# Kernel tuning notes

Hardware: AMD Instinct MI355X
Metric: run time of the kernel (lower is better)

Reference implementation:

```python
import jax, jax.numpy as jnp
import numpy as np

DIM = 256
HEADS = 4
DIM_HEADS = 32
HIDDEN = HEADS * DIM_HEADS


def setup_inputs() -> dict:
    key = jax.random.key(0)
    k0, k1, k2, k3, k4, k5, k6 = jax.random.split(key, 7)
    b, c, h, w = 16, DIM, 64, 64
    s = 1.0 / np.sqrt(DIM)
    return {
        "x": jax.random.normal(k0, (b, c, h, w), dtype=jnp.float32),
        "Wq": jax.random.normal(k1, (HIDDEN, DIM), dtype=jnp.float32) * s,
        "Wk": jax.random.normal(k2, (HIDDEN, DIM), dtype=jnp.float32) * s,
        "Wv": jax.random.normal(k3, (HIDDEN, DIM), dtype=jnp.float32) * s,
        "Wo": jax.random.normal(k4, (DIM, HIDDEN), dtype=jnp.float32) / np.sqrt(HIDDEN),
        "bo": jax.random.normal(k5, (DIM,), dtype=jnp.float32) * 0.01,
        "g": jnp.ones((DIM,), dtype=jnp.float32),
    }


def reference(x, Wq, Wk, Wv, Wo, bo, g):
    b, c, h, w = x.shape
    n = h * w
    scale = DIM_HEADS ** (-0.5)
    xf = x.reshape(b, c, n)  # [b,c,n]
    # 1x1 convs == channel matmuls
    q = jnp.einsum('dc,bcn->bdn', Wq, xf).reshape(b, HEADS, DIM_HEADS, n)
    k = jnp.einsum('dc,bcn->bdn', Wk, xf).reshape(b, HEADS, DIM_HEADS, n)
    v = jnp.einsum('dc,bcn->bdn', Wv, xf).reshape(b, HEADS, DIM_HEADS, n)
    q = jax.nn.softmax(q, axis=-2) * scale  # softmax over head-dim
    k = jax.nn.softmax(k, axis=-1)          # softmax over tokens
    v = v / n
    context = jnp.einsum('bhdn,bhen->bhde', k, v)  # [b,h,dh,dh]
    out = jnp.einsum('bhde,bhdn->bhen', context, q)  # [b,h,dh,n]
    out = out.reshape(b, HIDDEN, n)
    out = jnp.einsum('cd,bdn->bcn', Wo, out) + bo[None, :, None]
    # LayerNorm over channel dim (biased var, eps=1e-5 for fp32)
    eps = 1e-5
    mean = jnp.mean(out, axis=1, keepdims=True)
    var = jnp.var(out, axis=1, keepdims=True)
    out = (out - mean) * jax.lax.rsqrt(var + eps) * g[None, :, None]
    return out.reshape(b, c, h, w)
```

## Files before the change

kernel.cpp:

```cpp
#include <hip/hip_runtime.h>
#include <hip/hip_bf16.h>

typedef float f32x4 __attribute__((ext_vector_type(4)));
typedef short bf16x8 __attribute__((ext_vector_type(8)));
typedef unsigned short us4 __attribute__((ext_vector_type(4)));
typedef unsigned short us8 __attribute__((ext_vector_type(8)));

#define NB 16
#define NC 256
#define NTOK 4096
#define NHID 128

#define APAD 264
#define PK 68
#define PQ 132

__device__ __forceinline__ unsigned short f2bf(float f) {
  union { float f; unsigned u; } v; v.f = f;
  return (unsigned short)((v.u + 0x7fffu + ((v.u >> 16) & 1u)) >> 16);
}
__device__ __forceinline__ float bf2f(unsigned short h) {
  union { unsigned u; float f; } v; v.u = ((unsigned)h) << 16;
  return v.f;
}

__global__ __launch_bounds__(512) void k0_w(
    const float* __restrict__ Wq, const float* __restrict__ Wk,
    const float* __restrict__ Wv, unsigned short* __restrict__ Wswz)
{
  const int mt = blockIdx.x;
  const int t = threadIdx.x;
  const int ks = t >> 6, l = t & 63;
  const int m = mt * 16 + (l & 15);
  const int col = ks * 32 + (l >> 4) * 8;
  const float* src = (m < 128) ? (Wq + (size_t)m * NC)
                   : (m < 256) ? (Wk + (size_t)(m - 128) * NC)
                               : (Wv + (size_t)(m - 256) * NC);
  const float4 w0 = *(const float4*)(src + col);
  const float4 w1 = *(const float4*)(src + col + 4);
  us8 p;
  p[0] = f2bf(w0.x); p[1] = f2bf(w0.y); p[2] = f2bf(w0.z); p[3] = f2bf(w0.w);
  p[4] = f2bf(w1.x); p[5] = f2bf(w1.y); p[6] = f2bf(w1.z); p[7] = f2bf(w1.w);
  *(us8*)&Wswz[((size_t)(mt * 8 + ks)) * 512 + l * 8] = p;
}

__global__ __launch_bounds__(512, 4) void k1_qkv(
    const float* __restrict__ x, const unsigned short* __restrict__ Wswz,
    unsigned short* __restrict__ qswz, unsigned short* __restrict__ Pp,
    float* __restrict__ Sp)
{
  __shared__ __align__(16) unsigned char smem[51712];
  unsigned short* As = (unsigned short*)smem;
  unsigned short* postKV = (unsigned short*)smem;
  unsigned short* postQ = (unsigned short*)(smem + 34816);

  const int tile = blockIdx.x, b = blockIdx.y;
  const int n0 = tile * 64;
  const int t = threadIdx.x;
  const int wid = t >> 6, l = t & 63;
  const int l16 = l & 15, lhi = l >> 4;
  const int tokh = wid >> 2;
  const int mw = wid & 3;
  const int mb = mw * 96;

  {
    const int slot = t & 15;
    const int cp0 = t >> 4;
    const float* xb = x + ((size_t)b * NC) * NTOK + n0;
#pragma unroll
    for (int i = 0; i < 4; ++i) {
      const int c0 = 2 * (cp0 + 32 * i);
      const float4 a0 = *(const float4*)(xb + (size_t)c0 * NTOK + slot * 4);
      const float4 a1 = *(const float4*)(xb + (size_t)(c0 + 1) * NTOK + slot * 4);
      const float* p0 = (const float*)&a0;
      const float* p1 = (const float*)&a1;
#pragma unroll
      for (int j = 0; j < 4; ++j)
        *(unsigned*)&As[(slot * 4 + j) * APAD + c0] =
            (unsigned)f2bf(p0[j]) | ((unsigned)f2bf(p1[j]) << 16);
    }
  }
  __syncthreads();

  f32x4 acc[2][6];
#pragma unroll
  for (int i = 0; i < 2; ++i)
#pragma unroll
    for (int j = 0; j < 6; ++j) acc[i][j] = 0;

  const int mt0 = mw * 6;
  for (int ks = 0; ks < 8; ++ks) {
    bf16x8 af[2];
#pragma unroll
    for (int tf = 0; tf < 2; ++tf)
      af[tf] = *(const bf16x8*)&As[(tokh * 32 + tf * 16 + l16) * APAD + ks * 32 + lhi * 8];
#pragma unroll
    for (int nf = 0; nf < 6; ++nf) {
      const bf16x8 bfv = *(const bf16x8*)&Wswz[((size_t)((mt0 + nf) * 8 + ks)) * 512 + l * 8];
#pragma unroll
      for (int tf = 0; tf < 2; ++tf)
        acc[tf][nf] = __builtin_amdgcn_mfma_f32_16x16x32_bf16(af[tf], bfv, acc[tf][nf], 0, 0, 0);
    }
  }

  const float qscale = 0.1767766952966369f;
#pragma unroll
  for (int pr = 0; pr < 3; ++pr) {
    const int mg = mb + pr * 32;
    if (mg < 128) {
#pragma unroll
      for (int tf = 0; tf < 2; ++tf)
#pragma unroll
        for (int r = 0; r < 4; ++r) {
          const float a0 = acc[tf][2 * pr][r], a1 = acc[tf][2 * pr + 1][r];
          float mx = fmaxf(a0, a1);
          mx = fmaxf(mx, __shfl_xor(mx, 1));
          mx = fmaxf(mx, __shfl_xor(mx, 2));
          mx = fmaxf(mx, __shfl_xor(mx, 4));
          mx = fmaxf(mx, __shfl_xor(mx, 8));
          const float e0 = __expf(a0 - mx), e1 = __expf(a1 - mx);
          float s = e0 + e1;
          s += __shfl_xor(s, 1); s += __shfl_xor(s, 2);
          s += __shfl_xor(s, 4); s += __shfl_xor(s, 8);
          const float inv = qscale / s;
          acc[tf][2 * pr][r] = e0 * inv;
          acc[tf][2 * pr + 1][r] = e1 * inv;
        }
    } else if (mg < 256) {
#pragma unroll
      for (int f = 0; f < 2; ++f) {
        float s = 0.f;
#pragma unroll
        for (int tf = 0; tf < 2; ++tf)
#pragma unroll
          for (int r = 0; r < 4; ++r) {
            const float e = __expf(acc[tf][2 * pr + f][r]);
            acc[tf][2 * pr + f][r] = e;
            s += e;
          }
        s += __shfl_xor(s, 16);
        s += __shfl_xor(s, 32);
        if (l < 16)
          Sp[(((size_t)b * 64 + tile) * 2 + tokh) * 128 + (mg - 128) + f * 16 + l16] = s;
      }
    }
  }
  __syncthreads();

#pragma unroll
  for (int nf = 0; nf < 6; ++nf) {
    const int mg = mb + nf * 16;
    if (mg < 128) {
#pragma unroll
      for (int tf = 0; tf < 2; ++tf) {
        const int tok = tokh * 32 + tf * 16 + lhi * 4;
#pragma unroll
        for (int r = 0; r < 4; ++r)
          postQ[(tok + r) * PQ + mg + l16] = f2bf(acc[tf][nf][r]);
      }
    } else {
      const int row = mg - 128 + l16;
#pragma unroll
      for (int tf = 0; tf < 2; ++tf) {
        us4 p;
#pragma unroll
        for (int r = 0; r < 4; ++r) p[r] = f2bf(acc[tf][nf][r]);
        *(us4*)&postKV[row * PK + tokh * 32 + tf * 16 + lhi * 4] = p;
      }
    }
  }
  __syncthreads();

  if (wid >= 4) {
    const int h = wid - 4;
    f32x4 ca[2][2];
    ca[0][0] = 0; ca[0][1] = 0; ca[1][0] = 0; ca[1][1] = 0;
#pragma unroll
    for (int ks2 = 0; ks2 < 2; ++ks2) {
      bf16x8 ae[2], be[2];
#pragma unroll
      for (int d = 0; d < 2; ++d)
        ae[d] = *(const bf16x8*)&postKV[(h * 32 + d * 16 + l16) * PK + ks2 * 32 + lhi * 8];
#pragma unroll
      for (int e = 0; e < 2; ++e)
        be[e] = *(const bf16x8*)&postKV[(128 + h * 32 + e * 16 + l16) * PK + ks2 * 32 + lhi * 8];
#pragma unroll
      for (int d = 0; d < 2; ++d)
#pragma unroll
        for (int e = 0; e < 2; ++e)
          ca[d][e] = __builtin_amdgcn_mfma_f32_16x16x32_bf16(ae[d], be[e], ca[d][e], 0, 0, 0);
    }
    unsigned short* pb = Pp + (((size_t)b * 64 + tile) * 4 + h) * 1024;
#pragma unroll
    for (int d = 0; d < 2; ++d)
#pragma unroll
      for (int e = 0; e < 2; ++e) {
        us4 p;
#pragma unroll
        for (int r = 0; r < 4; ++r) p[r] = f2bf(ca[d][e][r]);
        *(us4*)&pb[(e * 16 + l16) * 32 + d * 16 + lhi * 4] = p;
      }
  } else {
    const int g = wid;
#pragma unroll
    for (int ks = 0; ks < 4; ++ks) {
      const bf16x8 v = *(const bf16x8*)&postQ[(g * 16 + l16) * PQ + ks * 32 + lhi * 8];
      *(bf16x8*)&qswz[(((size_t)(b * 256 + tile * 4 + g)) * 4 + ks) * 512 + l * 8] = v;
    }
  }
}

__global__ __launch_bounds__(256) void k2_reduce(
    const unsigned short* __restrict__ Pp, const float* __restrict__ Sp,
    float* __restrict__ Cn)
{
  __shared__ float Ss[32];
  const int h = blockIdx.x, b = blockIdx.y;
  const int t = threadIdx.x;
  if (t < 32) {
    float s = 0.f;
    const float* sb = Sp + (size_t)b * 16384 + h * 32 + t;
    for (int i = 0; i < 128; ++i) s += sb[i * 128];
    Ss[t] = 1.0f / (s * 4096.0f);
  }
  __syncthreads();
  const int e = t >> 3, d4 = (t & 7) * 4;
  f32x4 a = 0;
  for (int tile = 0; tile < 64; ++tile) {
    const us4 v = *(const us4*)&Pp[(((size_t)b * 64 + tile) * 4 + h) * 1024 + e * 32 + d4];
    a[0] += bf2f(v[0]); a[1] += bf2f(v[1]); a[2] += bf2f(v[2]); a[3] += bf2f(v[3]);
  }
  f32x4 o;
#pragma unroll
  for (int j = 0; j < 4; ++j) o[j] = a[j] * Ss[d4 + j];
  *(f32x4*)&Cn[(size_t)b * 4096 + h * 1024 + e * 32 + d4] = o;
}

__global__ __launch_bounds__(256) void k2_m(
    const float* __restrict__ Wo, const float* __restrict__ Cn,
    unsigned short* __restrict__ Mswz)
{
  const int ct = blockIdx.x, b = blockIdx.y;
  const int t = threadIdx.x;
  const int ks = t >> 6, l = t & 63;
  const int c = ct * 16 + (l & 15);
  const int d0 = (l >> 4) * 8;
  const float* wr = Wo + (size_t)c * NHID + ks * 32;
  const float* cb = Cn + (size_t)b * 4096 + ks * 1024;
  f32x4 s0 = 0, s1 = 0;
#pragma unroll 8
  for (int e = 0; e < 32; ++e) {
    const float w = wr[e];
    const f32x4 c0 = *(const f32x4*)&cb[e * 32 + d0];
    const f32x4 c1 = *(const f32x4*)&cb[e * 32 + d0 + 4];
#pragma unroll
    for (int j = 0; j < 4; ++j) { s0[j] += w * c0[j]; s1[j] += w * c1[j]; }
  }
  us8 p;
#pragma unroll
  for (int j = 0; j < 4; ++j) { p[j] = f2bf(s0[j]); p[4 + j] = f2bf(s1[j]); }
  *(us8*)&Mswz[(((size_t)b * 16 + ct) * 4 + ks) * 512 + l * 8] = p;
}

__global__ __launch_bounds__(256, 3) void k3_out(
    const unsigned short* __restrict__ qswz, const unsigned short* __restrict__ Mswz,
    const float* __restrict__ bo, const float* __restrict__ g, float* __restrict__ out)
{
  __shared__ float red[4 * 64 * 2];
  const int bx = blockIdx.x, b = blockIdx.y;
  const int t = threadIdx.x;
  const int wid = t >> 6, l = t & 63;
  const int l16 = l & 15, lhi = l >> 4;

  bf16x8 mf[4][4];
#pragma unroll
  for (int cf = 0; cf < 4; ++cf)
#pragma unroll
    for (int ks = 0; ks < 4; ++ks)
      mf[cf][ks] = *(const bf16x8*)&Mswz[(((size_t)b * 16 + wid * 4 + cf) * 4 + ks) * 512 + l * 8];

  f32x4 acc[4][4];
#pragma unroll
  for (int i = 0; i < 4; ++i)
#pragma unroll
    for (int j = 0; j < 4; ++j) acc[i][j] = 0;

#pragma unroll
  for (int tf = 0; tf < 4; ++tf) {
    bf16x8 qf[4];
#pragma unroll
    for (int ks = 0; ks < 4; ++ks)
      qf[ks] = *(const bf16x8*)&qswz[(((size_t)(b * 256 + bx * 4 + tf)) * 4 + ks) * 512 + l * 8];
#pragma unroll
    for (int ks = 0; ks < 4; ++ks)
#pragma unroll
      for (int cf = 0; cf < 4; ++cf)
        acc[tf][cf] = __builtin_amdgcn_mfma_f32_16x16x32_bf16(qf[ks], mf[cf][ks], acc[tf][cf], 0, 0, 0);
  }

  float bol[4], gl[4];
#pragma unroll
  for (int cf = 0; cf < 4; ++cf) {
    const int c = wid * 64 + cf * 16 + l16;
    bol[cf] = bo[c]; gl[cf] = g[c];
  }
#pragma unroll
  for (int tf = 0; tf < 4; ++tf)
#pragma unroll
    for (int cf = 0; cf < 4; ++cf)
#pragma unroll
      for (int r = 0; r < 4; ++r) acc[tf][cf][r] += bol[cf];

#pragma unroll
  for (int tf = 0; tf < 4; ++tf)
#pragma unroll
    for (int r = 0; r < 4; ++r) {
      float s = 0.f, q2 = 0.f;
#pragma unroll
      for (int cf = 0; cf < 4; ++cf) {
        const float v = acc[tf][cf][r];
        s += v; q2 += v * v;
      }
      s += __shfl_xor(s, 1); q2 += __shfl_xor(q2, 1);
      s += __shfl_xor(s, 2); q2 += __shfl_xor(q2, 2);
      s += __shfl_xor(s, 4); q2 += __shfl_xor(q2, 4);
      s += __shfl_xor(s, 8); q2 += __shfl_xor(q2, 8);
      if (l16 == 0) {
        const int tok = tf * 16 + lhi * 4 + r;
        red[(wid * 64 + tok) * 2] = s;
        red[(wid * 64 + tok) * 2 + 1] = q2;
      }
    }
  __syncthreads();

  float mean[4][4], rstd[4][4];
#pragma unroll
  for (int tf = 0; tf < 4; ++tf)
#pragma unroll
    for (int r = 0; r < 4; ++r) {
      const int tok = tf * 16 + lhi * 4 + r;
      float s = 0.f, q2 = 0.f;
#pragma unroll
      for (int cg = 0; cg < 4; ++cg) {
        s += red[(cg * 64 + tok) * 2];
        q2 += red[(cg * 64 + tok) * 2 + 1];
      }
      const float mu = s * (1.0f / 256.0f);
      const float var = q2 * (1.0f / 256.0f) - mu * mu;
      mean[tf][r] = mu;
      rstd[tf][r] = rsqrtf(var + 1e-5f);
    }

  float* ob = out + ((size_t)b * NC) * NTOK + bx * 64;
#pragma unroll
  for (int tf = 0; tf < 4; ++tf)
#pragma unroll
    for (int cf = 0; cf < 4; ++cf) {
      const int c = wid * 64 + cf * 16 + l16;
      f32x4 ov;
#pragma unroll
      for (int r = 0; r < 4; ++r)
        ov[r] = (acc[tf][cf][r] - mean[tf][r]) * rstd[tf][r] * gl[cf];
      *(f32x4*)&ob[(size_t)c * NTOK + tf * 16 + lhi * 4] = ov;
    }
}

extern "C" void kernel_launch(void* const* d_in, const int* in_sizes, int n_in,
                              void* d_out, int out_size, void* d_ws, size_t ws_size,
                              hipStream_t stream) {
  const float* x  = (const float*)d_in[0];
  const float* Wq = (const float*)d_in[1];
  const float* Wk = (const float*)d_in[2];
  const float* Wv = (const float*)d_in[3];
  const float* Wo = (const float*)d_in[4];
  const float* bo = (const float*)d_in[5];
  const float* g  = (const float*)d_in[6];
  float* out = (float*)d_out;

  char* ws = (char*)d_ws;
  unsigned short* Wswz = (unsigned short*)(ws);
  unsigned short* qswz = (unsigned short*)(ws + 262144);
  unsigned short* Pp   = (unsigned short*)(ws + 17039360);
  float*          Sp   = (float*)(ws + 25427968);
  float*          Cn   = (float*)(ws + 26476544);
  unsigned short* Mswz = (unsigned short*)(ws + 26738688);
  (void)ws_size; (void)in_sizes; (void)n_in; (void)out_size;

  hipLaunchKernelGGL(k0_w, dim3(24), dim3(512), 0, stream, Wq, Wk, Wv, Wswz);
  hipLaunchKernelGGL(k1_qkv, dim3(64, NB), dim3(512), 0, stream, x, Wswz, qswz, Pp, Sp);
  hipLaunchKernelGGL(k2_reduce, dim3(4, NB), dim3(256), 0, stream, Pp, Sp, Cn);
  hipLaunchKernelGGL(k2_m, dim3(16, NB), dim3(256), 0, stream, Wo, Cn, Mswz);
  hipLaunchKernelGGL(k3_out, dim3(64, NB), dim3(256), 0, stream, qswz, Mswz, bo, g, out);
}
```

Measured before the change: 92.16 us.

## Reassign QKV warp tiles, XOR-swizzle LDS layouts, use packed bf16 conversion

The QKV kernel now gives each warp all 64 tokens and three 16-row output fragments, so each Wswz fragment is fetched once per warp and the per-token-half split of key sums goes away. Padded LDS arrays are replaced by XOR-swizzled layouts, which shrink shared memory enough to raise the occupancy hint to 6 blocks. Manual bf16 rounding is replaced by the packed hardware conversion intrinsics. The risks are more accumulator registers per warp, which may not fit the new occupancy target, and an uneven softmax workload across warps.

```diff
diff --git a/kernel.cpp b/kernel.cpp
--- a/kernel.cpp
+++ b/kernel.cpp
@@ -4,20 +4,23 @@
 typedef float f32x4 __attribute__((ext_vector_type(4)));
 typedef short bf16x8 __attribute__((ext_vector_type(8)));
 typedef unsigned short us4 __attribute__((ext_vector_type(4)));
-typedef unsigned short us8 __attribute__((ext_vector_type(8)));
 
 #define NB 16
 #define NC 256
 #define NTOK 4096
 #define NHID 128
 
-#define APAD 264
-#define PK 68
-#define PQ 132
-
+__device__ __forceinline__ unsigned pk2(float lo, float hi) {
+  float2 f; f.x = lo; f.y = hi;
+  __hip_bfloat162 h = __float22bfloat162_rn(f);
+  unsigned u; __builtin_memcpy(&u, &h, 4); return u;
+}
 __device__ __forceinline__ unsigned short f2bf(float f) {
-  union { float f; unsigned u; } v; v.f = f;
-  return (unsigned short)((v.u + 0x7fffu + ((v.u >> 16) & 1u)) >> 16);
+  __hip_bfloat16 h = __float2bfloat16(f);
+  unsigned short u; __builtin_memcpy(&u, &h, 2); return u;
+}
+__device__ __forceinline__ uint2 pk4(f32x4 v) {
+  uint2 r; r.x = pk2(v[0], v[1]); r.y = pk2(v[2], v[3]); return r;
 }
 __device__ __forceinline__ float bf2f(unsigned short h) {
   union { unsigned u; float f; } v; v.u = ((unsigned)h) << 16;
@@ -38,30 +41,29 @@
                                : (Wv + (size_t)(m - 256) * NC);
   const float4 w0 = *(const float4*)(src + col);
   const float4 w1 = *(const float4*)(src + col + 4);
-  us8 p;
-  p[0] = f2bf(w0.x); p[1] = f2bf(w0.y); p[2] = f2bf(w0.z); p[3] = f2bf(w0.w);
-  p[4] = f2bf(w1.x); p[5] = f2bf(w1.y); p[6] = f2bf(w1.z); p[7] = f2bf(w1.w);
-  *(us8*)&Wswz[((size_t)(mt * 8 + ks)) * 512 + l * 8] = p;
-}
-
-__global__ __launch_bounds__(512, 4) void k1_qkv(
+  uint4 p;
+  p.x = pk2(w0.x, w0.y); p.y = pk2(w0.z, w0.w);
+  p.z = pk2(w1.x, w1.y); p.w = pk2(w1.z, w1.w);
+  *(uint4*)&Wswz[((size_t)(mt * 8 + ks)) * 512 + l * 8] = p;
+}
+
+__global__ __launch_bounds__(512, 6) void k1_qkv(
     const float* __restrict__ x, const unsigned short* __restrict__ Wswz,
     unsigned short* __restrict__ qswz, unsigned short* __restrict__ Pp,
     float* __restrict__ Sp)
 {
-  __shared__ __align__(16) unsigned char smem[51712];
-  unsigned short* As = (unsigned short*)smem;
-  unsigned short* postKV = (unsigned short*)smem;
-  unsigned short* postQ = (unsigned short*)(smem + 34816);
+  __shared__ __align__(16) unsigned char smem[49152];
 
   const int tile = blockIdx.x, b = blockIdx.y;
   const int n0 = tile * 64;
   const int t = threadIdx.x;
   const int wid = t >> 6, l = t & 63;
   const int l16 = l & 15, lhi = l >> 4;
-  const int tokh = wid >> 2;
-  const int mw = wid & 3;
-  const int mb = mw * 96;
+  const unsigned xr = (unsigned)((l16 & 7) << 4);
+
+  int fr[3];
+  if (wid < 4) { fr[0] = 2 * wid; fr[1] = 2 * wid + 1; fr[2] = 8 + wid; }
+  else { const int w = wid - 4; fr[0] = 12 + w; fr[1] = 16 + 2 * w; fr[2] = 17 + 2 * w; }
 
   {
     const int slot = t & 15;
@@ -75,98 +77,111 @@
       const float* p0 = (const float*)&a0;
       const float* p1 = (const float*)&a1;
 #pragma unroll
-      for (int j = 0; j < 4; ++j)
-        *(unsigned*)&As[(slot * 4 + j) * APAD + c0] =
-            (unsigned)f2bf(p0[j]) | ((unsigned)f2bf(p1[j]) << 16);
+      for (int j = 0; j < 4; ++j) {
+        const int tok = slot * 4 + j;
+        const unsigned off = (unsigned)(tok * 512 + 2 * c0) ^ ((unsigned)(tok & 7) << 4);
+        *(unsigned*)(smem + off) = pk2(p0[j], p1[j]);
+      }
     }
   }
   __syncthreads();
 
-  f32x4 acc[2][6];
-#pragma unroll
-  for (int i = 0; i < 2; ++i)
-#pragma unroll
-    for (int j = 0; j < 6; ++j) acc[i][j] = 0;
-
-  const int mt0 = mw * 6;
+  f32x4 acc[4][3];
+#pragma unroll
+  for (int i = 0; i < 4; ++i)
+#pragma unroll
+    for (int j = 0; j < 3; ++j) acc[i][j] = 0;
+
   for (int ks = 0; ks < 8; ++ks) {
-    bf16x8 af[2];
-#pragma unroll
-    for (int tf = 0; tf < 2; ++tf)
-      af[tf] = *(const bf16x8*)&As[(tokh * 32 + tf * 16 + l16) * APAD + ks * 32 + lhi * 8];
-#pragma unroll
-    for (int nf = 0; nf < 6; ++nf) {
-      const bf16x8 bfv = *(const bf16x8*)&Wswz[((size_t)((mt0 + nf) * 8 + ks)) * 512 + l * 8];
-#pragma unroll
-      for (int tf = 0; tf < 2; ++tf)
-        acc[tf][nf] = __builtin_amdgcn_mfma_f32_16x16x32_bf16(af[tf], bfv, acc[tf][nf], 0, 0, 0);
+    bf16x8 af[4];
+#pragma unroll
+    for (int tf = 0; tf < 4; ++tf)
+      af[tf] = *(const bf16x8*)(smem +
+          (((unsigned)((tf * 16 + l16) * 512 + ks * 64 + lhi * 16)) ^ xr));
+#pragma unroll
+    for (int f = 0; f < 3; ++f) {
+      const bf16x8 bfv = *(const bf16x8*)&Wswz[((size_t)(fr[f] * 8 + ks)) * 512 + l * 8];
+#pragma unroll
+      for (int tf = 0; tf < 4; ++tf)
+        acc[tf][f] = __builtin_amdgcn_mfma_f32_16x16x32_bf16(af[tf], bfv, acc[tf][f], 0, 0, 0);
     }
   }
 
   const float qscale = 0.1767766952966369f;
-#pragma unroll
-  for (int pr = 0; pr < 3; ++pr) {
-    const int mg = mb + pr * 32;
-    if (mg < 128) {
-#pragma unroll
-      for (int tf = 0; tf < 2; ++tf)
+  if (wid < 4) {
+#pragma unroll
+    for (int tf = 0; tf < 4; ++tf)
+#pragma unroll
+      for (int r = 0; r < 4; ++r) {
+        const float a0 = acc[tf][0][r], a1 = acc[tf][1][r];
+        float mx = fmaxf(a0, a1);
+        mx = fmaxf(mx, __shfl_xor(mx, 1));
+        mx = fmaxf(mx, __shfl_xor(mx, 2));
+        mx = fmaxf(mx, __shfl_xor(mx, 4));
+        mx = fmaxf(mx, __shfl_xor(mx, 8));
+        const float e0 = __expf(a0 - mx), e1 = __expf(a1 - mx);
+        float s = e0 + e1;
+        s += __shfl_xor(s, 1); s += __shfl_xor(s, 2);
+        s += __shfl_xor(s, 4); s += __shfl_xor(s, 8);
+        const float inv = qscale / s;
+        acc[tf][0][r] = e0 * inv;
+        acc[tf][1][r] = e1 * inv;
+      }
+    float s = 0.f;
+#pragma unroll
+    for (int tf = 0; tf < 4; ++tf)
+#pragma unroll
+      for (int r = 0; r < 4; ++r) {
+        const float e = __expf(acc[tf][2][r]);
+        acc[tf][2][r] = e;
+        s += e;
+      }
+    s += __shfl_xor(s, 16);
+    s += __shfl_xor(s, 32);
+    if (l < 16) Sp[((size_t)b * 64 + tile) * 128 + (fr[2] - 8) * 16 + l16] = s;
+  } else {
+    float s = 0.f;
+#pragma unroll
+    for (int tf = 0; tf < 4; ++tf)
+#pragma unroll
+      for (int r = 0; r < 4; ++r) {
+        const float e = __expf(acc[tf][0][r]);
+        acc[tf][0][r] = e;
+        s += e;
+      }
+    s += __shfl_xor(s, 16);
+    s += __shfl_xor(s, 32);
+    if (l < 16) Sp[((size_t)b * 64 + tile) * 128 + (fr[0] - 8) * 16 + l16] = s;
+  }
+  __syncthreads();
+
+  if (wid < 4) {
+#pragma unroll
+    for (int f = 0; f < 2; ++f) {
+      const int j = fr[f] * 16 + l16;
+#pragma unroll
+      for (int tf = 0; tf < 4; ++tf)
 #pragma unroll
         for (int r = 0; r < 4; ++r) {
-          const float a0 = acc[tf][2 * pr][r], a1 = acc[tf][2 * pr + 1][r];
-          float mx = fmaxf(a0, a1);
-          mx = fmaxf(mx, __shfl_xor(mx, 1));
-          mx = fmaxf(mx, __shfl_xor(mx, 2));
-          mx = fmaxf(mx, __shfl_xor(mx, 4));
-          mx = fmaxf(mx, __shfl_xor(mx, 8));
-          const float e0 = __expf(a0 - mx), e1 = __expf(a1 - mx);
-          float s = e0 + e1;
-          s += __shfl_xor(s, 1); s += __shfl_xor(s, 2);
-          s += __shfl_xor(s, 4); s += __shfl_xor(s, 8);
-          const float inv = qscale / s;
-          acc[tf][2 * pr][r] = e0 * inv;
-          acc[tf][2 * pr + 1][r] = e1 * inv;
+          const int tok = tf * 16 + lhi * 4 + r;
+          const unsigned off = 32768u + (unsigned)(tok * 256) +
+                               (((unsigned)(2 * j)) ^ ((unsigned)(tok & 7) << 4));
+          *(unsigned short*)(smem + off) = f2bf(acc[tf][f][r]);
         }
-    } else if (mg < 256) {
-#pragma unroll
-      for (int f = 0; f < 2; ++f) {
-        float s = 0.f;
-#pragma unroll
-        for (int tf = 0; tf < 2; ++tf)
-#pragma unroll
-          for (int r = 0; r < 4; ++r) {
-            const float e = __expf(acc[tf][2 * pr + f][r]);
-            acc[tf][2 * pr + f][r] = e;
-            s += e;
-          }
-        s += __shfl_xor(s, 16);
-        s += __shfl_xor(s, 32);
-        if (l < 16)
-          Sp[(((size_t)b * 64 + tile) * 2 + tokh) * 128 + (mg - 128) + f * 16 + l16] = s;
-      }
-    }
-  }
-  __syncthreads();
-
-#pragma unroll
-  for (int nf = 0; nf < 6; ++nf) {
-    const int mg = mb + nf * 16;
-    if (mg < 128) {
-#pragma unroll
-      for (int tf = 0; tf < 2; ++tf) {
-        const int tok = tokh * 32 + tf * 16 + lhi * 4;
-#pragma unroll
-        for (int r = 0; r < 4; ++r)
-          postQ[(tok + r) * PQ + mg + l16] = f2bf(acc[tf][nf][r]);
-      }
-    } else {
-      const int row = mg - 128 + l16;
-#pragma unroll
-      for (int tf = 0; tf < 2; ++tf) {
-        us4 p;
-#pragma unroll
-        for (int r = 0; r < 4; ++r) p[r] = f2bf(acc[tf][nf][r]);
-        *(us4*)&postKV[row * PK + tokh * 32 + tf * 16 + lhi * 4] = p;
-      }
+    }
+    const int row = (fr[2] - 8) * 16 + l16;
+#pragma unroll
+    for (int tf = 0; tf < 4; ++tf)
+      *(uint2*)(smem + (((unsigned)(row * 128 + tf * 32 + lhi * 8)) ^ xr)) = pk4(acc[tf][2]);
+  } else {
+    const int rowk = (fr[0] - 8) * 16 + l16;
+    const int rowv1 = 128 + (fr[1] - 16) * 16 + l16;
+    const int rowv2 = 128 + (fr[2] - 16) * 16 + l16;
+#pragma unroll
+    for (int tf = 0; tf < 4; ++tf) {
+      *(uint2*)(smem + (((unsigned)(rowk * 128 + tf * 32 + lhi * 8)) ^ xr)) = pk4(acc[tf][0]);
+      *(uint2*)(smem + (((unsigned)(rowv1 * 128 + tf * 32 + lhi * 8)) ^ xr)) = pk4(acc[tf][1]);
+      *(uint2*)(smem + (((unsigned)(rowv2 * 128 + tf * 32 + lhi * 8)) ^ xr)) = pk4(acc[tf][2]);
     }
   }
   __syncthreads();
@@ -180,10 +195,12 @@
       bf16x8 ae[2], be[2];
 #pragma unroll
       for (int d = 0; d < 2; ++d)
-        ae[d] = *(const bf16x8*)&postKV[(h * 32 + d * 16 + l16) * PK + ks2 * 32 + lhi * 8];
+        ae[d] = *(const bf16x8*)(smem +
+            (((unsigned)((h * 32 + d * 16 + l16) * 128 + ks2 * 64 + lhi * 16)) ^ xr));
 #pragma unroll
       for (int e = 0; e < 2; ++e)
-        be[e] = *(const bf16x8*)&postKV[(128 + h * 32 + e * 16 + l16) * PK + ks2 * 32 + lhi * 8];
+        be[e] = *(const bf16x8*)(smem +
+            (((unsigned)((128 + h * 32 + e * 16 + l16) * 128 + ks2 * 64 + lhi * 16)) ^ xr));
 #pragma unroll
       for (int d = 0; d < 2; ++d)
 #pragma unroll
@@ -194,17 +211,15 @@
 #pragma unroll
     for (int d = 0; d < 2; ++d)
 #pragma unroll
-      for (int e = 0; e < 2; ++e) {
-        us4 p;
-#pragma unroll
-        for (int r = 0; r < 4; ++r) p[r] = f2bf(ca[d][e][r]);
-        *(us4*)&pb[(e * 16 + l16) * 32 + d * 16 + lhi * 4] = p;
-      }
+      for (int e = 0; e < 2; ++e)
+        *(uint2*)&pb[(e * 16 + l16) * 32 + d * 16 + lhi * 4] = pk4(ca[d][e]);
   } else {
     const int g = wid;
+    const int tok = g * 16 + l16;
 #pragma unroll
     for (int ks = 0; ks < 4; ++ks) {
-      const bf16x8 v = *(const bf16x8*)&postQ[(g * 16 + l16) * PQ + ks * 32 + lhi * 8];
+      const bf16x8 v = *(const bf16x8*)(smem + 32768u + (unsigned)(tok * 256) +
+                          (((unsigned)(ks * 64 + lhi * 16)) ^ xr));
       *(bf16x8*)&qswz[(((size_t)(b * 256 + tile * 4 + g)) * 4 + ks) * 512 + l * 8] = v;
     }
   }
@@ -219,8 +234,8 @@
   const int t = threadIdx.x;
   if (t < 32) {
     float s = 0.f;
-    const float* sb = Sp + (size_t)b * 16384 + h * 32 + t;
-    for (int i = 0; i < 128; ++i) s += sb[i * 128];
+    const float* sb = Sp + (size_t)b * 64 * 128 + h * 32 + t;
+    for (int i = 0; i < 64; ++i) s += sb[i * 128];
     Ss[t] = 1.0f / (s * 4096.0f);
   }
   __syncthreads();
@@ -256,10 +271,10 @@
 #pragma unroll
     for (int j = 0; j < 4; ++j) { s0[j] += w * c0[j]; s1[j] += w * c1[j]; }
   }
-  us8 p;
-#pragma unroll
-  for (int j = 0; j < 4; ++j) { p[j] = f2bf(s0[j]); p[4 + j] = f2bf(s1[j]); }
-  *(us8*)&Mswz[(((size_t)b * 16 + ct) * 4 + ks) * 512 + l * 8] = p;
+  uint4 p;
+  p.x = pk2(s0[0], s0[1]); p.y = pk2(s0[2], s0[3]);
+  p.z = pk2(s1[0], s1[1]); p.w = pk2(s1[2], s1[3]);
+  *(uint4*)&Mswz[(((size_t)b * 16 + ct) * 4 + ks) * 512 + l * 8] = p;
 }
 
 __global__ __launch_bounds__(256, 3) void k3_out(
```

Result: slower. 113.2 us (+22.9%).
